# Kernel optimization log

Measured on AMD Instinct MI355X. Metric: run time of the kernel, lower is better.

The kernel has to match this reference:

```python
import jax, jax.numpy as jnp
import numpy as np

N_NODES = 50000
N_EDGES = 800000
DIM = 128
N_GRAPHS = 64
HEADS = 4
SCALE = (DIM // HEADS) ** -0.5
EPS = 1e-5
SLOPE = 0.01  # torch LeakyReLU default


def setup_inputs() -> dict:
    key = jax.random.key(0)
    ks = iter(jax.random.split(key, 48))
    def nrm(shape, s):
        return jax.random.normal(next(ks), shape, dtype=jnp.float32) * s
    inp = {
        "xA": nrm((N_NODES, DIM), 1.0),
        "xB": nrm((N_NODES, DIM), 1.0),
        "edge_index_A": jax.random.randint(next(ks), (2, N_EDGES), 0, N_NODES),
        "edge_index_B": jax.random.randint(next(ks), (2, N_EDGES), 0, N_NODES),
        # contiguous equal-size graph assignment (sorted, covers all B graphs)
        "batch_A": (jnp.arange(N_NODES) * N_GRAPHS) // N_NODES,
        "batch_B": (jnp.arange(N_NODES) * N_GRAPHS) // N_NODES,
    }
    s = DIM ** -0.5
    for name, shape in [("WA1", (DIM, DIM)), ("WA2", (DIM, DIM)),
                        ("WB1", (DIM, DIM)), ("WB2", (DIM, DIM)),
                        ("Wq", (DIM, DIM)), ("Wk", (DIM, DIM)),
                        ("Wv", (DIM, DIM)), ("Wo", (DIM, DIM)),
                        ("Wf1", (DIM, 2 * DIM)), ("Wf2", (2 * DIM, DIM)),
                        ("Wl1", (2 * DIM, DIM)), ("Wl2", (DIM, 1))]:
        inp[name] = nrm(shape, s)
    for name, shape in [("bA1", (DIM,)), ("bA2", (DIM,)), ("bB1", (DIM,)), ("bB2", (DIM,)),
                        ("bq", (DIM,)), ("bk", (DIM,)), ("bv", (DIM,)), ("bo", (DIM,)),
                        ("bf1", (2 * DIM,)), ("bf2", (DIM,)), ("bl1", (DIM,)), ("bl2", (1,))]:
        inp[name] = jnp.zeros(shape, jnp.float32)
    inp["g1"] = jnp.ones((DIM,), jnp.float32)
    inp["be1"] = jnp.zeros((DIM,), jnp.float32)
    inp["g2"] = jnp.ones((DIM,), jnp.float32)
    inp["be2"] = jnp.zeros((DIM,), jnp.float32)
    return inp


def _gcn(x, W, b, src, dst):
    # PyG GCNConv: XW, add self-loops, sym D^-1/2 (A+I) D^-1/2, scatter to dst, + bias
    h = x @ W
    deg = jax.ops.segment_sum(jnp.ones(src.shape, h.dtype), dst, N_NODES) + 1.0
    inv = jax.lax.rsqrt(deg)
    agg = jax.ops.segment_sum(h[src] * (inv[src] * inv[dst])[:, None], dst, N_NODES)
    return agg + h * (inv * inv)[:, None] + b  # self-loop term: norm_i^2 * h_i


def _encoder(x, edge_index, W1, b1, W2, b2):
    src, dst = edge_index[0], edge_index[1]
    h = jax.nn.leaky_relu(_gcn(x, W1, b1, src, dst), SLOPE)
    return _gcn(h, W2, b2, src, dst)  # dropout is identity in eval mode


def _pool(x, batch):
    s = jax.ops.segment_sum(x, batch, N_GRAPHS)
    c = jax.ops.segment_sum(jnp.ones((x.shape[0],), x.dtype), batch, N_GRAPHS)
    return s / c[:, None]


def _ln(x, g, b):
    m = x.mean(-1, keepdims=True)
    v = ((x - m) ** 2).mean(-1, keepdims=True)
    return (x - m) * jax.lax.rsqrt(v + EPS) * g + b


def reference(xA, xB, edge_index_A, edge_index_B, batch_A, batch_B,
              WA1, bA1, WA2, bA2, WB1, bB1, WB2, bB2,
              Wq, bq, Wk, bk, Wv, bv, Wo, bo,
              g1, be1, Wf1, bf1, Wf2, bf2, g2, be2,
              Wl1, bl1, Wl2, bl2):

    def cross(x_q, x_kv):
        Q = (x_q @ Wq + bq).reshape(-1, HEADS, DIM // HEADS)
        K = (x_kv @ Wk + bk).reshape(-1, HEADS, DIM // HEADS)
        V = (x_kv @ Wv + bv).reshape(-1, HEADS, DIM // HEADS)
        attn = jax.nn.softmax(jnp.einsum('qhd,khd->hqk', Q, K) * SCALE, axis=-1)
        out = jnp.einsum('hqk,khd->qhd', attn, V).reshape(x_q.shape[0], DIM)
        return out @ Wo + bo

    def block(x_q, x_kv):  # shared-weight CrossAttentionBlock (used both directions)
        x = _ln(x_q + cross(x_q, x_kv), g1, be1)
        ff = jax.nn.leaky_relu(x @ Wf1 + bf1, SLOPE) @ Wf2 + bf2
        return _ln(x + ff, g2, be2)

    gA = _encoder(xA, edge_index_A, WA1, bA1, WA2, bA2)
    gB = _encoder(xB, edge_index_B, WB1, bB1, WB2, bB2)
    hA = _pool(gA, batch_A)
    hB = _pool(gB, batch_B)
    hA_att = block(hA, hB)
    hB_att = block(hB, hA)
    h = jnp.concatenate([hA_att, hB_att], axis=-1)  # [B, 2*DIM]
    h = jax.nn.relu(h @ Wl1 + bl1)
    return h @ Wl2 + bl2  # [B, 1]
```

## Files before the change

### kernel.cpp

```cpp
#include <hip/hip_runtime.h>

#define N_NODESC 50000
#define N_EDGESC 800000
#define DIMC 128
#define NGC 64
#define HDC 32
#define SLOPEF 0.01f
#define EPSF 1e-5f
#define SCALEF 0.17677669529663687f

#define NBUK 782
#define KBLK 50
#define EPB 16000
#define GG 782
#define AG 12500

typedef __attribute__((ext_vector_type(8))) short bf16x8;
typedef __attribute__((ext_vector_type(4))) float f32x4;

static __device__ __forceinline__ unsigned short f2bf(float f) {
  unsigned u = __float_as_uint(f);
  u = u + 0x7FFFu + ((u >> 16) & 1u);
  return (unsigned short)(u >> 16);
}
static __device__ __forceinline__ float bf2f(unsigned short h) {
  return __uint_as_float(((unsigned)h) << 16);
}

__global__ __launch_bounds__(1024) void kbhist2(const int* __restrict__ eiA, const int* __restrict__ eiB,
                                                int* __restrict__ hist) {
  __shared__ int lh[NBUK];
  int side = blockIdx.x / KBLK, blk = blockIdx.x % KBLK;
  const int* ei = side ? eiB : eiA;
  int* hout = hist + side * KBLK * NBUK;
  int t = threadIdx.x;
  for (int i = t; i < NBUK; i += 1024) lh[i] = 0;
  __syncthreads();
  int e0 = blk * EPB;
  for (int e = e0 + t; e < e0 + EPB; e += 1024) {
    int d = ei[N_EDGESC + e];
    atomicAdd(&lh[d >> 6], 1);
  }
  __syncthreads();
  for (int i = t; i < NBUK; i += 1024) hout[blk * NBUK + i] = lh[i];
}

__global__ __launch_bounds__(1024) void kbscan2(const int* __restrict__ hist, int* __restrict__ bbase,
                                                int* __restrict__ bucket_base) {
  __shared__ int sd[1024];
  int side = blockIdx.x;
  const int* h = hist + side * KBLK * NBUK;
  int* bb = bbase + side * KBLK * NBUK;
  int* bub = bucket_base + side * (NBUK + 1);
  int t = threadIdx.x;
  int tot = 0;
  if (t < NBUK) {
    for (int k = 0; k < KBLK; ++k) tot += h[k * NBUK + t];
  }
  sd[t] = tot;
  __syncthreads();
  for (int off = 1; off < 1024; off <<= 1) {
    int u = (t >= off) ? sd[t - off] : 0;
    __syncthreads();
    sd[t] += u;
    __syncthreads();
  }
  if (t < NBUK) {
    int run = sd[t] - tot;
    bub[t] = run;
    for (int k = 0; k < KBLK; ++k) {
      bb[k * NBUK + t] = run;
      run += h[k * NBUK + t];
    }
  }
  if (t == 0) bub[NBUK] = N_EDGESC;
}

__global__ __launch_bounds__(1024) void kbin2(const int* __restrict__ eiA, const int* __restrict__ eiB,
                                              const int* __restrict__ bbase, unsigned* __restrict__ packed) {
  __shared__ int cur[NBUK];
  int side = blockIdx.x / KBLK, blk = blockIdx.x % KBLK;
  const int* ei = side ? eiB : eiA;
  const int* bb = bbase + side * KBLK * NBUK;
  unsigned* pk = packed + (size_t)side * N_EDGESC;
  int t = threadIdx.x;
  for (int i = t; i < NBUK; i += 1024) cur[i] = bb[blk * NBUK + i];
  __syncthreads();
  int e0 = blk * EPB;
  for (int e = e0 + t; e < e0 + EPB; e += 1024) {
    int s = ei[e];
    int d = ei[N_EDGESC + e];
    int b = d >> 6;
    int pos = atomicAdd(&cur[b], 1);
    pk[pos] = (unsigned)s | ((unsigned)(d & 63) << 16);
  }
}

__global__ __launch_bounds__(256) void kcsr2(const unsigned* __restrict__ packed, const int* __restrict__ bucket_base,
                                             unsigned short* __restrict__ csr16, int* __restrict__ rowptr,
                                             float* __restrict__ inv) {
  __shared__ int h64[64], o64[64], c64[64];
  int side = blockIdx.x / NBUK, b = blockIdx.x % NBUK;
  const unsigned* pk = packed + (size_t)side * N_EDGESC;
  const int* bub = bucket_base + side * (NBUK + 1);
  unsigned short* cs = csr16 + (size_t)side * N_EDGESC;
  int* rp = rowptr + side * (N_NODESC + 1);
  float* iv = inv + side * N_NODESC;
  int t = threadIdx.x;
  int beg = bub[b], end = bub[b + 1];
  if (t < 64) h64[t] = 0;
  __syncthreads();
  for (int e = beg + t; e < end; e += 256) atomicAdd(&h64[pk[e] >> 16], 1);
  __syncthreads();
  if (t == 0) {
    int run = 0;
    for (int j = 0; j < 64; ++j) { o64[j] = run; run += h64[j]; }
  }
  __syncthreads();
  if (t < 64) c64[t] = o64[t];
  __syncthreads();
  for (int e = beg + t; e < end; e += 256) {
    unsigned p = pk[e];
    int pos = atomicAdd(&c64[p >> 16], 1);
    cs[beg + pos] = (unsigned short)(p & 0xFFFFu);
  }
  if (t < 64) {
    int node = b * 64 + t;
    if (node < N_NODESC) {
      rp[node] = beg + o64[t];
      iv[node] = rsqrtf((float)h64[t] + 1.0f);
    }
  }
  if (b == NBUK - 1 && t == 0) rp[N_NODESC] = N_EDGESC;
}

__global__ __launch_bounds__(256) void wconv(const float* __restrict__ W0, const float* __restrict__ W1,
                                             const float* __restrict__ W2, const float* __restrict__ W3,
                                             unsigned short* __restrict__ Wt) {
  int m = blockIdx.x >> 4;
  int idx = (blockIdx.x & 15) * 256 + threadIdx.x;
  int fs = idx >> 6, lane = idx & 63;
  int ks = fs >> 3, nf = fs & 7;
  int n = nf * 16 + (lane & 15);
  int k0 = ks * 32 + (lane >> 4) * 8;
  const float* W = (m == 0) ? W0 : (m == 1) ? W1 : (m == 2) ? W2 : W3;
  unsigned short* hi = Wt + (size_t)m * 128 * 512 + (size_t)(fs * 2) * 512 + lane * 8;
  bf16x8 vh, vl;
#pragma unroll
  for (int j = 0; j < 8; ++j) {
    float a = W[(k0 + j) * DIMC + n];
    unsigned short h = f2bf(a);
    vh[j] = (short)h;
    vl[j] = (short)f2bf(a - bf2f(h));
  }
  *(bf16x8*)hi = vh;
  *(bf16x8*)(hi + 512) = vl;
}

__global__ __launch_bounds__(256) void gemm_l1(const float* __restrict__ xA, const float* __restrict__ xB,
                                               const unsigned short* __restrict__ Wt, const float* __restrict__ inv,
                                               unsigned short* __restrict__ H) {
  __shared__ unsigned short lds[64 * 136];
  int side = blockIdx.x / GG, lb = blockIdx.x % GG;
  const float* X = side ? xB : xA;
  const unsigned short* Wm = Wt + (size_t)(side * 2) * 128 * 512;
  const float* iv = inv + side * N_NODESC;
  unsigned short* Y = H + (size_t)side * N_NODESC * DIMC;
  int wave = threadIdx.x >> 6, lane = threadIdx.x & 63;
  int l15 = lane & 15, kb = lane >> 4;
  int row0 = lb * 64 + wave * 16;
  int rA = row0 + l15;
  const bool valid = rA < N_NODESC;
  f32x4 acc[8];
#pragma unroll
  for (int nf = 0; nf < 8; ++nf) acc[nf] = 0.f;
#pragma unroll
  for (int ks = 0; ks < 4; ++ks) {
    int kbase = ks * 32 + kb * 8;
    bf16x8 a;
    if (valid) {
      const float* xp = &X[(size_t)rA * DIMC + kbase];
      float4 x0 = *(const float4*)xp;
      float4 x1 = *(const float4*)(xp + 4);
      a[0] = (short)f2bf(x0.x); a[1] = (short)f2bf(x0.y);
      a[2] = (short)f2bf(x0.z); a[3] = (short)f2bf(x0.w);
      a[4] = (short)f2bf(x1.x); a[5] = (short)f2bf(x1.y);
      a[6] = (short)f2bf(x1.z); a[7] = (short)f2bf(x1.w);
    } else {
      a = (short)0;
    }
    const unsigned short* wp = Wm + (size_t)(ks * 16) * 512 + lane * 8;
#pragma unroll
    for (int nf = 0; nf < 8; ++nf) {
      bf16x8 bh = *(const bf16x8*)(wp + (nf * 2) * 512);
      bf16x8 bl = *(const bf16x8*)(wp + (nf * 2 + 1) * 512);
      acc[nf] = __builtin_amdgcn_mfma_f32_16x16x32_bf16(a, bh, acc[nf], 0, 0, 0);
      acc[nf] = __builtin_amdgcn_mfma_f32_16x16x32_bf16(a, bl, acc[nf], 0, 0, 0);
    }
  }
  int lrow = wave * 16 + kb * 4;
#pragma unroll
  for (int r = 0; r < 4; ++r) {
    int rr = row0 + kb * 4 + r;
    float s = (rr < N_NODESC) ? iv[rr] : 0.f;
#pragma unroll
    for (int nf = 0; nf < 8; ++nf) {
      lds[(lrow + r) * 136 + nf * 16 + l15] = f2bf(acc[nf][r] * s);
    }
  }
  __syncthreads();
  int tr = threadIdx.x >> 2, c0 = (threadIdx.x & 3) * 32;
  int grow = lb * 64 + tr;
  if (grow < N_NODESC) {
#pragma unroll
    for (int i = 0; i < 4; ++i) {
      *(uint4*)&Y[(size_t)grow * DIMC + c0 + i * 8] = *(const uint4*)&lds[tr * 136 + c0 + i * 8];
    }
  }
}

__global__ __launch_bounds__(256) void gemm_l2(const unsigned short* __restrict__ Gb,
                                               const unsigned short* __restrict__ Wt, const float* __restrict__ inv,
                                               unsigned short* __restrict__ H) {
  __shared__ unsigned short lds[64 * 136];
  int side = blockIdx.x / GG, lb = blockIdx.x % GG;
  const unsigned short* X = Gb + (size_t)side * N_NODESC * DIMC;
  const unsigned short* Wm = Wt + (size_t)(side * 2 + 1) * 128 * 512;
  const float* iv = inv + side * N_NODESC;
  unsigned short* Y = H + (size_t)side * N_NODESC * DIMC;
  int wave = threadIdx.x >> 6, lane = threadIdx.x & 63;
  int l15 = lane & 15, kb = lane >> 4;
  int row0 = lb * 64 + wave * 16;
  int rA = row0 + l15;
  const bool valid = rA < N_NODESC;
  f32x4 acc[8];
#pragma unroll
  for (int nf = 0; nf < 8; ++nf) acc[nf] = 0.f;
#pragma unroll
  for (int ks = 0; ks < 4; ++ks) {
    int kbase = ks * 32 + kb * 8;
    bf16x8 a;
    if (valid) {
      a = *(const bf16x8*)&X[(size_t)rA * DIMC + kbase];
    } else {
      a = (short)0;
    }
    const unsigned short* wp = Wm + (size_t)(ks * 16) * 512 + lane * 8;
#pragma unroll
    for (int nf = 0; nf < 8; ++nf) {
      bf16x8 bh = *(const bf16x8*)(wp + (nf * 2) * 512);
      bf16x8 bl = *(const bf16x8*)(wp + (nf * 2 + 1) * 512);
      acc[nf] = __builtin_amdgcn_mfma_f32_16x16x32_bf16(a, bh, acc[nf], 0, 0, 0);
      acc[nf] = __builtin_amdgcn_mfma_f32_16x16x32_bf16(a, bl, acc[nf], 0, 0, 0);
    }
  }
  int lrow = wave * 16 + kb * 4;
#pragma unroll
  for (int r = 0; r < 4; ++r) {
    int rr = row0 + kb * 4 + r;
    float s = (rr < N_NODESC) ? iv[rr] : 0.f;
#pragma unroll
    for (int nf = 0; nf < 8; ++nf) {
      lds[(lrow + r) * 136 + nf * 16 + l15] = f2bf(acc[nf][r] * s);
    }
  }
  __syncthreads();
  int tr = threadIdx.x >> 2, c0 = (threadIdx.x & 3) * 32;
  int grow = lb * 64 + tr;
  if (grow < N_NODESC) {
#pragma unroll
    for (int i = 0; i < 4; ++i) {
      *(uint4*)&Y[(size_t)grow * DIMC + c0 + i * 8] = *(const uint4*)&lds[tr * 136 + c0 + i * 8];
    }
  }
}

__global__ __launch_bounds__(256) void agg12(const unsigned short* __restrict__ H, const float* __restrict__ inv,
                                             const int* __restrict__ rowptr, const unsigned short* __restrict__ csr16,
                                             const float* __restrict__ biasA, const float* __restrict__ biasB,
                                             unsigned short* __restrict__ G, int do_relu) {
  int side = blockIdx.x / AG, lb = blockIdx.x % AG;
  int node = lb * 4 + (threadIdx.x >> 6);
  if (node >= N_NODESC) return;
  const unsigned short* Hs = H + (size_t)side * N_NODESC * DIMC;
  const float* iv = inv + side * N_NODESC;
  const int* rp = rowptr + side * (N_NODESC + 1);
  const unsigned short* csr = csr16 + (size_t)side * N_EDGESC;
  const float* bias = side ? biasB : biasA;
  unsigned short* out = G + (size_t)side * N_NODESC * DIMC;
  int lane = threadIdx.x & 63;
  int cg = (lane & 31) * 4;
  int slot = lane >> 5;
  int beg = rp[node], end = rp[node + 1];
  float4 acc = make_float4(0.f, 0.f, 0.f, 0.f);
  int e = beg;
  for (; e + 8 <= end; e += 8) {
    int s0 = csr[e + slot];
    int s1 = csr[e + 2 + slot];
    int s2 = csr[e + 4 + slot];
    int s3 = csr[e + 6 + slot];
    ushort4 v0 = *(const ushort4*)&Hs[(size_t)s0 * DIMC + cg];
    ushort4 v1 = *(const ushort4*)&Hs[(size_t)s1 * DIMC + cg];
    ushort4 v2 = *(const ushort4*)&Hs[(size_t)s2 * DIMC + cg];
    ushort4 v3 = *(const ushort4*)&Hs[(size_t)s3 * DIMC + cg];
    acc.x += (bf2f(v0.x) + bf2f(v1.x)) + (bf2f(v2.x) + bf2f(v3.x));
    acc.y += (bf2f(v0.y) + bf2f(v1.y)) + (bf2f(v2.y) + bf2f(v3.y));
    acc.z += (bf2f(v0.z) + bf2f(v1.z)) + (bf2f(v2.z) + bf2f(v3.z));
    acc.w += (bf2f(v0.w) + bf2f(v1.w)) + (bf2f(v2.w) + bf2f(v3.w));
  }
  for (int t = e + slot; t < end; t += 2) {
    int s = csr[t];
    ushort4 v = *(const ushort4*)&Hs[(size_t)s * DIMC + cg];
    acc.x += bf2f(v.x); acc.y += bf2f(v.y); acc.z += bf2f(v.z); acc.w += bf2f(v.w);
  }
  acc.x += __shfl_xor(acc.x, 32, 64);
  acc.y += __shfl_xor(acc.y, 32, 64);
  acc.z += __shfl_xor(acc.z, 32, 64);
  acc.w += __shfl_xor(acc.w, 32, 64);
  if (slot == 0) {
    ushort4 sv = *(const ushort4*)&Hs[(size_t)node * DIMC + cg];
    float sc = iv[node];
    float4 b = *(const float4*)&bias[cg];
    float4 o;
    o.x = (acc.x + bf2f(sv.x)) * sc + b.x;
    o.y = (acc.y + bf2f(sv.y)) * sc + b.y;
    o.z = (acc.z + bf2f(sv.z)) * sc + b.z;
    o.w = (acc.w + bf2f(sv.w)) * sc + b.w;
    if (do_relu) {
      o.x = (o.x > 0.f) ? o.x : SLOPEF * o.x;
      o.y = (o.y > 0.f) ? o.y : SLOPEF * o.y;
      o.z = (o.z > 0.f) ? o.z : SLOPEF * o.z;
      o.w = (o.w > 0.f) ? o.w : SLOPEF * o.w;
    }
    ushort4 ob;
    ob.x = f2bf(o.x); ob.y = f2bf(o.y); ob.z = f2bf(o.z); ob.w = f2bf(o.w);
    *(ushort4*)&out[(size_t)node * DIMC + cg] = ob;
  }
}

__global__ __launch_bounds__(128) void pool2(const unsigned short* __restrict__ G,
                                             const int* __restrict__ batA, const int* __restrict__ batB,
                                             float* __restrict__ psA, float* __restrict__ psB,
                                             int* __restrict__ pcA, int* __restrict__ pcB) {
  int side = blockIdx.x / GG, lb = blockIdx.x % GG;
  const unsigned short* g = G + (size_t)side * N_NODESC * DIMC;
  const int* batch = side ? batB : batA;
  float* psum = side ? psB : psA;
  int* pcnt = side ? pcB : pcA;
  int t = threadIdx.x;
  int n0 = lb * 64;
  int nend = min(n0 + 64, N_NODESC);
  int cur = batch[n0];
  float acc = 0.f;
  int c = 0;
  for (int n = n0; n < nend; ++n) {
    int b = batch[n];
    if (b != cur) {
      atomicAdd(&psum[cur * DIMC + t], acc);
      if (t == 0) atomicAdd(&pcnt[cur], c);
      acc = 0.f;
      c = 0;
      cur = b;
    }
    acc += bf2f(g[(size_t)n * DIMC + t]);
    c += 1;
  }
  atomicAdd(&psum[cur * DIMC + t], acc);
  if (t == 0) atomicAdd(&pcnt[cur], c);
}

__global__ __launch_bounds__(128) void mean_kernel(const float* __restrict__ psA, const int* __restrict__ pcA,
                                                   const float* __restrict__ psB, const int* __restrict__ pcB,
                                                   float* __restrict__ hA, float* __restrict__ hB) {
  int dir = blockIdx.x >> 6, g = blockIdx.x & 63, t = threadIdx.x;
  const float* ps = dir ? psB : psA;
  const int* pc = dir ? pcB : pcA;
  float* h = dir ? hB : hA;
  h[g * DIMC + t] = ps[g * DIMC + t] / (float)max(pc[g], 1);
}

__global__ __launch_bounds__(128) void qkv_kernel(const float* __restrict__ hA, const float* __restrict__ hB,
                                                  const float* __restrict__ Wq, const float* __restrict__ bq,
                                                  const float* __restrict__ Wk, const float* __restrict__ bk,
                                                  const float* __restrict__ Wv, const float* __restrict__ bv,
                                                  float* __restrict__ Q0, float* __restrict__ K0, float* __restrict__ V0,
                                                  float* __restrict__ Q1, float* __restrict__ K1, float* __restrict__ V1) {
  __shared__ float xs[DIMC];
  int task = blockIdx.x >> 6, r = blockIdx.x & 63, t = threadIdx.x;
  const float *X, *W, *b;
  float* Y;
  switch (task) {
    case 0: X = hA; W = Wq; b = bq; Y = Q0; break;
    case 1: X = hB; W = Wk; b = bk; Y = K0; break;
    case 2: X = hB; W = Wv; b = bv; Y = V0; break;
    case 3: X = hB; W = Wq; b = bq; Y = Q1; break;
    case 4: X = hA; W = Wk; b = bk; Y = K1; break;
    default: X = hA; W = Wv; b = bv; Y = V1; break;
  }
  xs[t] = X[r * DIMC + t];
  __syncthreads();
  float acc = b[t];
  for (int k = 0; k < DIMC; ++k) acc += xs[k] * W[k * DIMC + t];
  Y[r * DIMC + t] = acc;
}

__global__ __launch_bounds__(64) void attn_kernel(const float* __restrict__ Q0, const float* __restrict__ K0,
                                                  const float* __restrict__ V0, const float* __restrict__ Q1,
                                                  const float* __restrict__ K1, const float* __restrict__ V1,
                                                  float* __restrict__ O0, float* __restrict__ O1) {
  __shared__ float ps[64];
  int b = blockIdx.x;
  int dir = b >> 8, h = (b >> 6) & 3, q = b & 63;
  const float* Q = dir ? Q1 : Q0;
  const float* K = dir ? K1 : K0;
  const float* V = dir ? V1 : V0;
  float* O = dir ? O1 : O0;
  int k = threadIdx.x;
  const float* qp = Q + q * DIMC + h * HDC;
  const float* kp = K + k * DIMC + h * HDC;
  float s = 0.f;
#pragma unroll
  for (int d = 0; d < HDC; ++d) s += qp[d] * kp[d];
  s *= SCALEF;
  float m = s;
#pragma unroll
  for (int off = 32; off >= 1; off >>= 1) m = fmaxf(m, __shfl_xor(m, off, 64));
  float p = __expf(s - m);
  float sum = p;
#pragma unroll
  for (int off = 32; off >= 1; off >>= 1) sum += __shfl_xor(sum, off, 64);
  p /= sum;
  ps[k] = p;
  __syncthreads();
  int half = k >> 5, d = k & 31;
  float acc = 0.f;
#pragma unroll
  for (int j = 0; j < 32; ++j) {
    int kk = half * 32 + j;
    acc += ps[kk] * V[kk * DIMC + h * HDC + d];
  }
  acc += __shfl_xor(acc, 32, 64);
  if (half == 0) O[q * DIMC + h * HDC + d] = acc;
}

__device__ inline float blk_sum128(float v, float* red) {
#pragma unroll
  for (int off = 32; off >= 1; off >>= 1) v += __shfl_xor(v, off, 64);
  if ((threadIdx.x & 63) == 0) red[threadIdx.x >> 6] = v;
  __syncthreads();
  float r = red[0] + red[1];
  __syncthreads();
  return r;
}

__global__ __launch_bounds__(128) void oln_kernel(const float* __restrict__ O0, const float* __restrict__ O1,
                                                  const float* __restrict__ hA, const float* __restrict__ hB,
                                                  const float* __restrict__ Wo, const float* __restrict__ bo,
                                                  const float* __restrict__ g1, const float* __restrict__ be1,
                                                  float* __restrict__ X0, float* __restrict__ X1) {
  __shared__ float os[DIMC];
  __shared__ float red[2];
  int dir = blockIdx.x >> 6, q = blockIdx.x & 63, t = threadIdx.x;
  const float* O = dir ? O1 : O0;
  const float* xq = dir ? hB : hA;
  float* Xo = dir ? X1 : X0;
  os[t] = O[q * DIMC + t];
  __syncthreads();
  float acc = bo[t] + xq[q * DIMC + t];
  for (int k = 0; k < DIMC; ++k) acc += os[k] * Wo[k * DIMC + t];
  float mean = blk_sum128(acc, red) * (1.f / DIMC);
  float d = acc - mean;
  float var = blk_sum128(d * d, red) * (1.f / DIMC);
  Xo[q * DIMC + t] = d * rsqrtf(var + EPSF) * g1[t] + be1[t];
}

__global__ __launch_bounds__(256) void ff1_kernel(const float* __restrict__ X0, const float* __restrict__ X1,
                                                  const float* __restrict__ Wf1, const float* __restrict__ bf1,
                                                  float* __restrict__ F0, float* __restrict__ F1) {
  __shared__ float xs[DIMC];
  int dir = blockIdx.x >> 6, q = blockIdx.x & 63, t = threadIdx.x;
  const float* X = dir ? X1 : X0;
  float* F = dir ? F1 : F0;
  if (t < DIMC) xs[t] = X[q * DIMC + t];
  __syncthreads();
  float acc = bf1[t];
  for (int k = 0; k < DIMC; ++k) acc += xs[k] * Wf1[k * 256 + t];
  acc = (acc > 0.f) ? acc : SLOPEF * acc;
  F[q * 256 + t] = acc;
}

__global__ __launch_bounds__(128) void ffln_kernel(const float* __restrict__ F0, const float* __restrict__ F1,
                                                   const float* __restrict__ X0, const float* __restrict__ X1,
                                                   const float* __restrict__ Wf2, const float* __restrict__ bf2,
                                                   const float* __restrict__ g2, const float* __restrict__ be2,
                                                   float* __restrict__ Y0, float* __restrict__ Y1) {
  __shared__ float fs[256];
  __shared__ float red[2];
  int dir = blockIdx.x >> 6, q = blockIdx.x & 63, t = threadIdx.x;
  const float* F = dir ? F1 : F0;
  const float* X = dir ? X1 : X0;
  float* Y = dir ? Y1 : Y0;
  fs[t] = F[q * 256 + t];
  fs[t + 128] = F[q * 256 + t + 128];
  __syncthreads();
  float acc = bf2[t] + X[q * DIMC + t];
  for (int k = 0; k < 256; ++k) acc += fs[k] * Wf2[k * DIMC + t];
  float mean = blk_sum128(acc, red) * (1.f / DIMC);
  float d = acc - mean;
  float var = blk_sum128(d * d, red) * (1.f / DIMC);
  Y[q * DIMC + t] = d * rsqrtf(var + EPSF) * g2[t] + be2[t];
}

__global__ __launch_bounds__(128) void head_kernel(const float* __restrict__ Y0, const float* __restrict__ Y1,
                                                   const float* __restrict__ Wl1, const float* __restrict__ bl1,
                                                   const float* __restrict__ Wl2, const float* __restrict__ bl2,
                                                   float* __restrict__ out) {
  __shared__ float cs[256];
  __shared__ float red[2];
  int g = blockIdx.x, t = threadIdx.x;
  cs[t] = Y0[g * DIMC + t];
  cs[t + 128] = Y1[g * DIMC + t];
  __syncthreads();
  float acc = bl1[t];
  for (int k = 0; k < 256; ++k) acc += cs[k] * Wl1[k * DIMC + t];
  acc = fmaxf(acc, 0.f);
  float s = blk_sum128(acc * Wl2[t], red);
  if (t == 0) out[g] = s + bl2[0];
}

extern "C" void kernel_launch(void* const* d_in, const int* in_sizes, int n_in,
                              void* d_out, int out_size, void* d_ws, size_t ws_size,
                              hipStream_t stream) {
  const float* xA = (const float*)d_in[0];
  const float* xB = (const float*)d_in[1];
  const int* eiA = (const int*)d_in[2];
  const int* eiB = (const int*)d_in[3];
  const int* batA = (const int*)d_in[4];
  const int* batB = (const int*)d_in[5];
  const float* WA1 = (const float*)d_in[6];
  const float* WA2 = (const float*)d_in[7];
  const float* WB1 = (const float*)d_in[8];
  const float* WB2 = (const float*)d_in[9];
  const float* Wq = (const float*)d_in[10];
  const float* Wk = (const float*)d_in[11];
  const float* Wv = (const float*)d_in[12];
  const float* Wo = (const float*)d_in[13];
  const float* Wf1 = (const float*)d_in[14];
  const float* Wf2 = (const float*)d_in[15];
  const float* Wl1 = (const float*)d_in[16];
  const float* Wl2 = (const float*)d_in[17];
  const float* bA1 = (const float*)d_in[18];
  const float* bA2 = (const float*)d_in[19];
  const float* bB1 = (const float*)d_in[20];
  const float* bB2 = (const float*)d_in[21];
  const float* bq = (const float*)d_in[22];
  const float* bk = (const float*)d_in[23];
  const float* bv = (const float*)d_in[24];
  const float* bo = (const float*)d_in[25];
  const float* bf1 = (const float*)d_in[26];
  const float* bf2 = (const float*)d_in[27];
  const float* bl1 = (const float*)d_in[28];
  const float* bl2 = (const float*)d_in[29];
  const float* g1 = (const float*)d_in[30];
  const float* be1 = (const float*)d_in[31];
  const float* g2 = (const float*)d_in[32];
  const float* be2 = (const float*)d_in[33];

  char* base = (char*)d_ws;
  size_t off = 0;
  auto alloc = [&](size_t bytes) -> char* {
    char* r = base + off;
    off += (bytes + 255) & ~(size_t)255;
    return r;
  };
  unsigned short* h_buf = (unsigned short*)alloc((size_t)2 * N_NODESC * DIMC * 2);
  unsigned short* g_buf = (unsigned short*)alloc((size_t)2 * N_NODESC * DIMC * 2);
  unsigned* packed = (unsigned*)alloc((size_t)2 * N_EDGESC * 4);
  unsigned short* csr16 = (unsigned short*)alloc((size_t)2 * N_EDGESC * 2);
  int* rowptr = (int*)alloc((size_t)2 * (N_NODESC + 1) * 4);
  float* inv = (float*)alloc((size_t)2 * N_NODESC * 4);
  int* hist = (int*)alloc((size_t)2 * KBLK * NBUK * 4);
  int* bbase = (int*)alloc((size_t)2 * KBLK * NBUK * 4);
  int* bucket_base = (int*)alloc((size_t)2 * (NBUK + 1) * 4);
  unsigned short* wtbuf = (unsigned short*)alloc((size_t)4 * 128 * 512 * 2);
  size_t poff0 = off;
  float* psA = (float*)alloc(NGC * DIMC * 4);
  float* psB = (float*)alloc(NGC * DIMC * 4);
  int* pcA = (int*)alloc(NGC * 4);
  int* pcB = (int*)alloc(NGC * 4);
  size_t pbytes = off - poff0;
  float* mhA = (float*)alloc(NGC * DIMC * 4);
  float* mhB = (float*)alloc(NGC * DIMC * 4);
  float* Q0 = (float*)alloc(NGC * DIMC * 4);
  float* K0 = (float*)alloc(NGC * DIMC * 4);
  float* V0 = (float*)alloc(NGC * DIMC * 4);
  float* Q1 = (float*)alloc(NGC * DIMC * 4);
  float* K1 = (float*)alloc(NGC * DIMC * 4);
  float* V1 = (float*)alloc(NGC * DIMC * 4);
  float* O0 = (float*)alloc(NGC * DIMC * 4);
  float* O1 = (float*)alloc(NGC * DIMC * 4);
  float* X0 = (float*)alloc(NGC * DIMC * 4);
  float* X1 = (float*)alloc(NGC * DIMC * 4);
  float* F0 = (float*)alloc(NGC * 256 * 4);
  float* F1 = (float*)alloc(NGC * 256 * 4);
  float* Y0 = (float*)alloc(NGC * DIMC * 4);
  float* Y1 = (float*)alloc(NGC * DIMC * 4);

  hipMemsetAsync(base + poff0, 0, pbytes, stream);
  wconv<<<64, 256, 0, stream>>>(WA1, WA2, WB1, WB2, wtbuf);

  kbhist2<<<2 * KBLK, 1024, 0, stream>>>(eiA, eiB, hist);
  kbscan2<<<2, 1024, 0, stream>>>(hist, bbase, bucket_base);
  kbin2<<<2 * KBLK, 1024, 0, stream>>>(eiA, eiB, bbase, packed);
  kcsr2<<<2 * NBUK, 256, 0, stream>>>(packed, bucket_base, csr16, rowptr, inv);

  gemm_l1<<<2 * GG, 256, 0, stream>>>(xA, xB, wtbuf, inv, h_buf);
  agg12<<<2 * AG, 256, 0, stream>>>(h_buf, inv, rowptr, csr16, bA1, bB1, g_buf, 1);
  gemm_l2<<<2 * GG, 256, 0, stream>>>(g_buf, wtbuf, inv, h_buf);
  agg12<<<2 * AG, 256, 0, stream>>>(h_buf, inv, rowptr, csr16, bA2, bB2, g_buf, 0);
  pool2<<<2 * GG, 128, 0, stream>>>(g_buf, batA, batB, psA, psB, pcA, pcB);

  mean_kernel<<<128, 128, 0, stream>>>(psA, pcA, psB, pcB, mhA, mhB);
  qkv_kernel<<<384, 128, 0, stream>>>(mhA, mhB, Wq, bq, Wk, bk, Wv, bv, Q0, K0, V0, Q1, K1, V1);
  attn_kernel<<<512, 64, 0, stream>>>(Q0, K0, V0, Q1, K1, V1, O0, O1);
  oln_kernel<<<128, 128, 0, stream>>>(O0, O1, mhA, mhB, Wo, bo, g1, be1, X0, X1);
  ff1_kernel<<<128, 256, 0, stream>>>(X0, X1, Wf1, bf1, F0, F1);
  ffln_kernel<<<128, 128, 0, stream>>>(F0, F1, X0, X1, Wf2, bf2, g2, be2, Y0, Y1);
  head_kernel<<<64, 128, 0, stream>>>(Y0, Y1, Wl1, bl1, Wl2, bl2, (float*)d_out);
}
```

Measured before the change: 295.6 us.

## Store GCN hidden features in FP8 to halve gather traffic in aggregation

The GEMM epilogues now pack the scaled hidden features into FP8 (e4m3), with a fixed x16 prescale to keep values in range. The aggregation kernel gathers one 32-bit word per lane instead of four bf16 values, unpacks them, and undoes the scale. This halves the bytes moved by the random neighbour gathers that dominate aggregation. In exchange it costs accuracy from FP8 quantisation and adds conversion work, with a software fallback if the hardware conversion builtins are missing.

```diff
diff --git a/kernel.cpp b/kernel.cpp
--- a/kernel.cpp
+++ b/kernel.cpp
@@ -17,6 +17,7 @@
 
 typedef __attribute__((ext_vector_type(8))) short bf16x8;
 typedef __attribute__((ext_vector_type(4))) float f32x4;
+typedef __attribute__((ext_vector_type(2))) float f32x2;
 
 static __device__ __forceinline__ unsigned short f2bf(float f) {
   unsigned u = __float_as_uint(f);
@@ -25,6 +26,57 @@
 }
 static __device__ __forceinline__ float bf2f(unsigned short h) {
   return __uint_as_float(((unsigned)h) << 16);
+}
+
+#if defined(__has_builtin)
+#if __has_builtin(__builtin_amdgcn_cvt_pk_f32_fp8) && __has_builtin(__builtin_amdgcn_cvt_pk_fp8_f32)
+#define HW_FP8 1
+#endif
+#endif
+#ifndef HW_FP8
+#define HW_FP8 0
+#endif
+
+static __device__ __forceinline__ unsigned enc_fp8(float x) {
+  unsigned u = __float_as_uint(x);
+  unsigned s = (u >> 24) & 0x80u;
+  unsigned mag = u & 0x7FFFFFFFu;
+  if (mag >= 0x43E00000u) return s | 0x7Eu;
+  unsigned r = mag + 0x7FFFFu + ((mag >> 20) & 1u);
+  int e8 = (int)(r >> 23) - 120;
+  if (e8 <= 0) {
+    float ax = __uint_as_float(mag);
+    int m = (int)(ax * 512.0f + 0.5f);
+    if (m > 7) m = 7;
+    return s | (unsigned)m;
+  }
+  return s | ((unsigned)e8 << 3) | ((r >> 20) & 7u);
+}
+static __device__ __forceinline__ float dec_fp8(unsigned b) {
+  unsigned em = b & 0x7Fu;
+  float mag = (em >= 8) ? __uint_as_float((em << 20) + 0x3C000000u)
+                        : (float)em * 0.001953125f;
+  return (b & 0x80u) ? -mag : mag;
+}
+static __device__ __forceinline__ unsigned pk_fp8x4(float a, float b, float c, float d) {
+#if HW_FP8
+  int v = 0;
+  v = __builtin_amdgcn_cvt_pk_fp8_f32(a, b, v, false);
+  v = __builtin_amdgcn_cvt_pk_fp8_f32(c, d, v, true);
+  return (unsigned)v;
+#else
+  return enc_fp8(a) | (enc_fp8(b) << 8) | (enc_fp8(c) << 16) | (enc_fp8(d) << 24);
+#endif
+}
+static __device__ __forceinline__ float4 upk_fp8x4(unsigned v) {
+#if HW_FP8
+  f32x2 lo = __builtin_amdgcn_cvt_pk_f32_fp8((int)v, false);
+  f32x2 hi = __builtin_amdgcn_cvt_pk_f32_fp8((int)v, true);
+  return make_float4(lo[0], lo[1], hi[0], hi[1]);
+#else
+  return make_float4(dec_fp8(v & 0xFF), dec_fp8((v >> 8) & 0xFF),
+                     dec_fp8((v >> 16) & 0xFF), dec_fp8(v >> 24));
+#endif
 }
 
 __global__ __launch_bounds__(1024) void kbhist2(const int* __restrict__ eiA, const int* __restrict__ eiB,
@@ -157,15 +209,28 @@
   *(bf16x8*)(hi + 512) = vl;
 }
 
+static __device__ __forceinline__ void epi_store_fp8(const unsigned short* lds, unsigned* Y, int lb) {
+  int tr = threadIdx.x >> 2, q = threadIdx.x & 3;
+  int grow = lb * 64 + tr;
+  if (grow >= N_NODESC) return;
+#pragma unroll
+  for (int i = 0; i < 8; ++i) {
+    int col = (q + 4 * i) * 4;
+    ushort4 v = *(const ushort4*)&lds[tr * 136 + col];
+    unsigned pk = pk_fp8x4(bf2f(v.x), bf2f(v.y), bf2f(v.z), bf2f(v.w));
+    Y[(size_t)grow * 32 + q + 4 * i] = pk;
+  }
+}
+
 __global__ __launch_bounds__(256) void gemm_l1(const float* __restrict__ xA, const float* __restrict__ xB,
                                                const unsigned short* __restrict__ Wt, const float* __restrict__ inv,
-                                               unsigned short* __restrict__ H) {
+                                               unsigned* __restrict__ H) {
   __shared__ unsigned short lds[64 * 136];
   int side = blockIdx.x / GG, lb = blockIdx.x % GG;
   const float* X = side ? xB : xA;
   const unsigned short* Wm = Wt + (size_t)(side * 2) * 128 * 512;
   const float* iv = inv + side * N_NODESC;
-  unsigned short* Y = H + (size_t)side * N_NODESC * DIMC;
+  unsigned* Y = H + (size_t)side * N_NODESC * 32;
   int wave = threadIdx.x >> 6, lane = threadIdx.x & 63;
   int l15 = lane & 15, kb = lane >> 4;
   int row0 = lb * 64 + wave * 16;
@@ -202,32 +267,25 @@
 #pragma unroll
   for (int r = 0; r < 4; ++r) {
     int rr = row0 + kb * 4 + r;
-    float s = (rr < N_NODESC) ? iv[rr] : 0.f;
+    float s = (rr < N_NODESC) ? iv[rr] * 16.0f : 0.f;
 #pragma unroll
     for (int nf = 0; nf < 8; ++nf) {
       lds[(lrow + r) * 136 + nf * 16 + l15] = f2bf(acc[nf][r] * s);
     }
   }
   __syncthreads();
-  int tr = threadIdx.x >> 2, c0 = (threadIdx.x & 3) * 32;
-  int grow = lb * 64 + tr;
-  if (grow < N_NODESC) {
-#pragma unroll
-    for (int i = 0; i < 4; ++i) {
-      *(uint4*)&Y[(size_t)grow * DIMC + c0 + i * 8] = *(const uint4*)&lds[tr * 136 + c0 + i * 8];
-    }
-  }
+  epi_store_fp8(lds, Y, lb);
 }
 
 __global__ __launch_bounds__(256) void gemm_l2(const unsigned short* __restrict__ Gb,
                                                const unsigned short* __restrict__ Wt, const float* __restrict__ inv,
-                                               unsigned short* __restrict__ H) {
+                                               unsigned* __restrict__ H) {
   __shared__ unsigned short lds[64 * 136];
   int side = blockIdx.x / GG, lb = blockIdx.x % GG;
   const unsigned short* X = Gb + (size_t)side * N_NODESC * DIMC;
   const unsigned short* Wm = Wt + (size_t)(side * 2 + 1) * 128 * 512;
   const float* iv = inv + side * N_NODESC;
-  unsigned short* Y = H + (size_t)side * N_NODESC * DIMC;
+  unsigned* Y = H + (size_t)side * N_NODESC * 32;
   int wave = threadIdx.x >> 6, lane = threadIdx.x & 63;
   int l15 = lane & 15, kb = lane >> 4;
   int row0 = lb * 64 + wave * 16;
@@ -258,38 +316,31 @@
 #pragma unroll
   for (int r = 0; r < 4; ++r) {
     int rr = row0 + kb * 4 + r;
-    float s = (rr < N_NODESC) ? iv[rr] : 0.f;
+    float s = (rr < N_NODESC) ? iv[rr] * 16.0f : 0.f;
 #pragma unroll
     for (int nf = 0; nf < 8; ++nf) {
       lds[(lrow + r) * 136 + nf * 16 + l15] = f2bf(acc[nf][r] * s);
     }
   }
   __syncthreads();
-  int tr = threadIdx.x >> 2, c0 = (threadIdx.x & 3) * 32;
-  int grow = lb * 64 + tr;
-  if (grow < N_NODESC) {
-#pragma unroll
-    for (int i = 0; i < 4; ++i) {
-      *(uint4*)&Y[(size_t)grow * DIMC + c0 + i * 8] = *(const uint4*)&lds[tr * 136 + c0 + i * 8];
-    }
-  }
-}
-
-__global__ __launch_bounds__(256) void agg12(const unsigned short* __restrict__ H, const float* __restrict__ inv,
+  epi_store_fp8(lds, Y, lb);
+}
+
+__global__ __launch_bounds__(256) void agg12(const unsigned* __restrict__ H, const float* __restrict__ inv,
                                              const int* __restrict__ rowptr, const unsigned short* __restrict__ csr16,
                                              const float* __restrict__ biasA, const float* __restrict__ biasB,
                                              unsigned short* __restrict__ G, int do_relu) {
   int side = blockIdx.x / AG, lb = blockIdx.x % AG;
   int node = lb * 4 + (threadIdx.x >> 6);
   if (node >= N_NODESC) return;
-  const unsigned short* Hs = H + (size_t)side * N_NODESC * DIMC;
+  const unsigned* Hp = H + (size_t)side * N_NODESC * 32;
   const float* iv = inv + side * N_NODESC;
   const int* rp = rowptr + side * (N_NODESC + 1);
   const unsigned short* csr = csr16 + (size_t)side * N_EDGESC;
   const float* bias = side ? biasB : biasA;
   unsigned short* out = G + (size_t)side * N_NODESC * DIMC;
   int lane = threadIdx.x & 63;
-  int cg = (lane & 31) * 4;
+  int ug = lane & 31;
   int slot = lane >> 5;
   int beg = rp[node], end = rp[node + 1];
   float4 acc = make_float4(0.f, 0.f, 0.f, 0.f);
@@ -299,33 +350,38 @@
     int s1 = csr[e + 2 + slot];
     int s2 = csr[e + 4 + slot];
     int s3 = csr[e + 6 + slot];
-    ushort4 v0 = *(const ushort4*)&Hs[(size_t)s0 * DIMC + cg];
-    ushort4 v1 = *(const ushort4*)&Hs[(size_t)s1 * DIMC + cg];
-    ushort4 v2 = *(const ushort4*)&Hs[(size_t)s2 * DIMC + cg];
-    ushort4 v3 = *(const ushort4*)&Hs[(size_t)s3 * DIMC + cg];
-    acc.x += (bf2f(v0.x) + bf2f(v1.x)) + (bf2f(v2.x) + bf2f(v3.x));
-    acc.y += (bf2f(v0.y) + bf2f(v1.y)) + (bf2f(v2.y) + bf2f(v3.y));
-    acc.z += (bf2f(v0.z) + bf2f(v1.z)) + (bf2f(v2.z) + bf2f(v3.z));
-    acc.w += (bf2f(v0.w) + bf2f(v1.w)) + (bf2f(v2.w) + bf2f(v3.w));
+    unsigned u0 = Hp[(size_t)s0 * 32 + ug];
+    unsigned u1 = Hp[(size_t)s1 * 32 + ug];
+    unsigned u2 = Hp[(size_t)s2 * 32 + ug];
+    unsigned u3 = Hp[(size_t)s3 * 32 + ug];
+    float4 v0 = upk_fp8x4(u0);
+    float4 v1 = upk_fp8x4(u1);
+    float4 v2 = upk_fp8x4(u2);
+    float4 v3 = upk_fp8x4(u3);
+    acc.x += (v0.x + v1.x) + (v2.x + v3.x);
+    acc.y += (v0.y + v1.y) + (v2.y + v3.y);
+    acc.z += (v0.z + v1.z) + (v2.z + v3.z);
+    acc.w += (v0.w + v1.w) + (v2.w + v3.w);
   }
   for (int t = e + slot; t < end; t += 2) {
     int s = csr[t];
-    ushort4 v = *(const ushort4*)&Hs[(size_t)s * DIMC + cg];
-    acc.x += bf2f(v.x); acc.y += bf2f(v.y); acc.z += bf2f(v.z); acc.w += bf2f(v.w);
+    float4 v = upk_fp8x4(Hp[(size_t)s * 32 + ug]);
+    acc.x += v.x; acc.y += v.y; acc.z += v.z; acc.w += v.w;
   }
   acc.x += __shfl_xor(acc.x, 32, 64);
   acc.y += __shfl_xor(acc.y, 32, 64);
   acc.z += __shfl_xor(acc.z, 32, 64);
   acc.w += __shfl_xor(acc.w, 32, 64);
   if (slot == 0) {
-    ushort4 sv = *(const ushort4*)&Hs[(size_t)node * DIMC + cg];
-    float sc = iv[node];
-    float4 b = *(const float4*)&bias[cg];
+    float4 sv = upk_fp8x4(Hp[(size_t)node * 32 + ug]);
+    float sc = iv[node] * 0.0625f;
+    const float* bp = &bias[ug * 4];
+    float4 b = *(const float4*)bp;
     float4 o;
-    o.x = (acc.x + bf2f(sv.x)) * sc + b.x;
-    o.y = (acc.y + bf2f(sv.y)) * sc + b.y;
-    o.z = (acc.z + bf2f(sv.z)) * sc + b.z;
-    o.w = (acc.w + bf2f(sv.w)) * sc + b.w;
+    o.x = (acc.x + sv.x) * sc + b.x;
+    o.y = (acc.y + sv.y) * sc + b.y;
+    o.z = (acc.z + sv.z) * sc + b.z;
+    o.w = (acc.w + sv.w) * sc + b.w;
     if (do_relu) {
       o.x = (o.x > 0.f) ? o.x : SLOPEF * o.x;
       o.y = (o.y > 0.f) ? o.y : SLOPEF * o.y;
@@ -334,7 +390,7 @@
     }
     ushort4 ob;
     ob.x = f2bf(o.x); ob.y = f2bf(o.y); ob.z = f2bf(o.z); ob.w = f2bf(o.w);
-    *(ushort4*)&out[(size_t)node * DIMC + cg] = ob;
+    *(ushort4*)&out[(size_t)node * DIMC + ug * 4] = ob;
   }
 }
 
@@ -573,7 +629,7 @@
     off += (bytes + 255) & ~(size_t)255;
     return r;
   };
-  unsigned short* h_buf = (unsigned short*)alloc((size_t)2 * N_NODESC * DIMC * 2);
+  unsigned* h_buf = (unsigned*)alloc((size_t)2 * N_NODESC * 32 * 4);
   unsigned short* g_buf = (unsigned short*)alloc((size_t)2 * N_NODESC * DIMC * 2);
   unsigned* packed = (unsigned*)alloc((size_t)2 * N_EDGESC * 4);
   unsigned short* csr16 = (unsigned short*)alloc((size_t)2 * N_EDGESC * 2);
```

Result: faster. 268.0 us (-9.3%).
